# Performance work log

Measured on AMD Instinct MI355X. Metric: run time of the kernel, lower is better.

The kernel has to match this reference:

```python
import math
import jax, jax.numpy as jnp
import numpy as np

S, B, D, MAX_LEN, P = 4096, 64, 256, 4096, 8


def _sinusoid_pe(max_len, dim):
    pos = np.arange(max_len, dtype=np.float32)[:, None]
    div = np.exp(np.arange(0, dim, 2, dtype=np.float32) * (-math.log(10000.0) / dim))
    pe = np.zeros((max_len, dim), dtype=np.float32)
    pe[:, 0::2] = np.sin(pos * div)
    pe[:, 1::2] = np.cos(pos * div)
    return jnp.asarray(pe)[:, None, :]  # [max_len, 1, dim]


def setup_inputs() -> dict:
    key = jax.random.key(0)
    k1, k2, k3 = jax.random.split(key, 3)
    x = jax.random.normal(k1, (S, B, D), dtype=jnp.float32)
    peak_positions = jax.random.randint(k2, (B, P), 0, S)  # int indices into seq axis
    pe = _sinusoid_pe(MAX_LEN, D)
    table = jax.random.normal(k3, (MAX_LEN, D), dtype=jnp.float32) * 0.02  # embedding weights
    return {"x": x, "peak_positions": peak_positions, "pe": pe, "table": table}


def reference(x, peak_positions, pe, table):
    seq_len, batch, dim = x.shape
    x = x + pe[:seq_len]  # broadcast [S,1,D] over batch
    # valid peaks: 0 <= p < seq_len; invalid contribute zero
    mask = (peak_positions >= 0) & (peak_positions < seq_len)  # [B,P]
    idx = jnp.where(mask, peak_positions, 0)  # safe gather index
    emb = table[idx] * mask[..., None].astype(x.dtype)  # [B,P,D]
    bidx = jnp.broadcast_to(jnp.arange(batch)[:, None], idx.shape)  # [B,P]
    # scatter-add embeddings at (peak_idx, batch) positions; duplicates accumulate
    peak_sum = jnp.zeros_like(x).at[idx, bidx].add(emb)
    return x + peak_sum
```

## Files before the change

kernel.cpp:

```cpp
#include <hip/hip_runtime.h>

#define S_LEN 4096
#define BATCH 64
#define DIM 256
#define NPEAK 8

__global__ void pe_add_kernel(const float4* __restrict__ x,
                              const float4* __restrict__ pe,
                              float4* __restrict__ out,
                              int total4) {
    int tid = blockIdx.x * blockDim.x + threadIdx.x;
    int stride = gridDim.x * blockDim.x;
    const int row4 = BATCH * DIM / 4;
    const int d4n = DIM / 4;
    for (int i = tid; i < total4; i += stride) {
        int s = i / row4;
        int d4 = i % d4n;
        float4 xv = x[i];
        float4 pv = pe[s * d4n + d4];
        float4 o;
        o.x = xv.x + pv.x;
        o.y = xv.y + pv.y;
        o.z = xv.z + pv.z;
        o.w = xv.w + pv.w;
        out[i] = o;
    }
}

__global__ void peak_scatter_kernel(const int* __restrict__ peaks,
                                    const float* __restrict__ table,
                                    float* __restrict__ out) {
    int bp = blockIdx.x;
    int b = bp / NPEAK;
    int p = peaks[bp];
    if (p < 0 || p >= S_LEN) return;
    int d = threadIdx.x;
    size_t off = (size_t)p * (BATCH * DIM) + (size_t)b * DIM + d;
    atomicAdd(&out[off], table[(size_t)p * DIM + d]);
}

extern "C" void kernel_launch(void* const* d_in, const int* in_sizes, int n_in,
                              void* d_out, int out_size, void* d_ws, size_t ws_size,
                              hipStream_t stream) {
    const float* x     = (const float*)d_in[0];
    const int* peaks   = (const int*)d_in[1];
    const float* pe    = (const float*)d_in[2];
    const float* table = (const float*)d_in[3];
    float* out = (float*)d_out;

    const int total4 = S_LEN * BATCH * DIM / 4;
    const int block = 256;
    int grid = (total4 + block - 1) / block;
    if (grid > 2048) grid = 2048;

    pe_add_kernel<<<grid, block, 0, stream>>>(
        (const float4*)x, (const float4*)pe, (float4*)out, total4);

    peak_scatter_kernel<<<BATCH * NPEAK, DIM, 0, stream>>>(peaks, table, out);
}
```

Baseline: 110.7 us.

## Fuse positional-encoding add and peak scatter into one streaming kernel

Replaces the two-kernel sequence (elementwise PE add followed by an atomic scatter of table rows) with a single grid-stride kernel. Each thread caches its batch's peak positions in registers and adds count*table[s] inline when the current sequence index matches a peak. This removes the second launch and its atomics. It also uses nontemporal loads and stores on the large x and out streams. The fusion relies on the grid stride being a multiple of the per-sequence row size, so each thread's batch and column index stay fixed.

```diff
diff --git a/kernel.cpp b/kernel.cpp
--- a/kernel.cpp
+++ b/kernel.cpp
@@ -4,39 +4,41 @@
 #define BATCH 64
 #define DIM 256
 #define NPEAK 8
+#define TOTAL4 (S_LEN * BATCH * DIM / 4)
 
-__global__ void pe_add_kernel(const float4* __restrict__ x,
-                              const float4* __restrict__ pe,
-                              float4* __restrict__ out,
-                              int total4) {
-    int tid = blockIdx.x * blockDim.x + threadIdx.x;
-    int stride = gridDim.x * blockDim.x;
-    const int row4 = BATCH * DIM / 4;
-    const int d4n = DIM / 4;
-    for (int i = tid; i < total4; i += stride) {
-        int s = i / row4;
-        int d4 = i % d4n;
-        float4 xv = x[i];
-        float4 pv = pe[s * d4n + d4];
-        float4 o;
-        o.x = xv.x + pv.x;
-        o.y = xv.y + pv.y;
-        o.z = xv.z + pv.z;
-        o.w = xv.w + pv.w;
-        out[i] = o;
+typedef float f32x4 __attribute__((ext_vector_type(4)));
+
+__global__ __launch_bounds__(256) void fused_pe_peak_kernel(
+    const f32x4* __restrict__ x,
+    const int*   __restrict__ peaks,
+    const f32x4* __restrict__ pe,
+    const f32x4* __restrict__ table,
+    f32x4* __restrict__ out)
+{
+    const int tid = blockIdx.x * blockDim.x + threadIdx.x;
+    const int stride = gridDim.x * blockDim.x;
+    const int b  = (tid >> 6) & (BATCH - 1);
+    const int d4 = tid & (DIM / 4 - 1);
+
+    int pk[NPEAK];
+    #pragma unroll
+    for (int j = 0; j < NPEAK; ++j) pk[j] = peaks[b * NPEAK + j];
+
+    for (int i = tid; i < TOTAL4; i += stride) {
+        const int s = i >> 12;
+        f32x4 xv = __builtin_nontemporal_load(&x[i]);
+        f32x4 pv = pe[(s << 6) + d4];
+        f32x4 o = xv + pv;
+
+        int cnt = 0;
+        #pragma unroll
+        for (int j = 0; j < NPEAK; ++j) cnt += (pk[j] == s) ? 1 : 0;
+        if (cnt) {
+            f32x4 tv = table[(s << 6) + d4];
+            o += (float)cnt * tv;
+        }
+        __builtin_nontemporal_store(o, &out[i]);
     }
-}
-
-__global__ void peak_scatter_kernel(const int* __restrict__ peaks,
-                                    const float* __restrict__ table,
-                                    float* __restrict__ out) {
-    int bp = blockIdx.x;
-    int b = bp / NPEAK;
-    int p = peaks[bp];
-    if (p < 0 || p >= S_LEN) return;
-    int d = threadIdx.x;
-    size_t off = (size_t)p * (BATCH * DIM) + (size_t)b * DIM + d;
-    atomicAdd(&out[off], table[(size_t)p * DIM + d]);
 }
 
 extern "C" void kernel_launch(void* const* d_in, const int* in_sizes, int n_in,
@@ -46,15 +48,8 @@
     const int* peaks   = (const int*)d_in[1];
     const float* pe    = (const float*)d_in[2];
     const float* table = (const float*)d_in[3];
-    float* out = (float*)d_out;
 
-    const int total4 = S_LEN * BATCH * DIM / 4;
-    const int block = 256;
-    int grid = (total4 + block - 1) / block;
-    if (grid > 2048) grid = 2048;
-
-    pe_add_kernel<<<grid, block, 0, stream>>>(
-        (const float4*)x, (const float4*)pe, (float4*)out, total4);
-
-    peak_scatter_kernel<<<BATCH * NPEAK, DIM, 0, stream>>>(peaks, table, out);
+    fused_pe_peak_kernel<<<2048, 256, 0, stream>>>(
+        (const f32x4*)x, peaks, (const f32x4*)pe, (const f32x4*)table,
+        (f32x4*)d_out);
 }
```

Measured after the change: 104.1 us. 1.06x faster.
